# Performance work log

Hardware: AMD Instinct MI355X
Metric: run time of the kernel (lower is better)

## Reference

```python
import jax, jax.numpy as jnp
import numpy as np

DIM = 1024
EPS = 1e-5


def setup_inputs() -> dict:
    key = jax.random.key(0)
    ks = jax.random.split(key, 7)
    C = DIM
    x = jax.random.normal(ks[0], (4, 4096, C), dtype=jnp.float32)
    norm_w = jnp.ones((C,), dtype=jnp.float32)
    norm_b = jnp.zeros((C,), dtype=jnp.float32)
    s = 1.0 / np.sqrt(C)
    qkv_w = jax.random.uniform(ks[1], (3 * C, C), dtype=jnp.float32, minval=-s, maxval=s)
    qkv_b = jax.random.uniform(ks[2], (3 * C,), dtype=jnp.float32, minval=-s, maxval=s)
    proj_w = jax.random.uniform(ks[3], (C, C), dtype=jnp.float32, minval=-s, maxval=s)
    proj_b = jax.random.uniform(ks[4], (C,), dtype=jnp.float32, minval=-s, maxval=s)
    return {"x": x, "norm_w": norm_w, "norm_b": norm_b, "qkv_w": qkv_w,
            "qkv_b": qkv_b, "proj_w": proj_w, "proj_b": proj_b}


def _layernorm(x, w, b):
    mu = jnp.mean(x, axis=-1, keepdims=True)
    var = jnp.mean(jnp.square(x - mu), axis=-1, keepdims=True)
    return (x - mu) * jax.lax.rsqrt(var + EPS) * w + b


def reference(x, norm_w, norm_b, qkv_w, qkv_b, proj_w, proj_b):
    B, T, C = x.shape
    residual = x
    h = _layernorm(x, norm_w, norm_b)
    qkv = jnp.einsum('btc,oc->bto', h, qkv_w) + qkv_b  # [B,T,3C]
    q, k, v = qkv[..., :C], qkv[..., C:2 * C], qkv[..., 2 * C:]
    attn = jnp.einsum('btc,bsc->bts', q, k) / jnp.sqrt(jnp.float32(C))  # raw QK^T, no softmax
    o = jnp.einsum('bts,bsc->btc', attn, v)
    o = jnp.einsum('btc,oc->bto', o, proj_w) + proj_b
    return residual + o  # dropout is identity in eval mode
```

## Files before the change

### kernel.cpp

```cpp
#include <hip/hip_runtime.h>

typedef _Float16 f16;
typedef _Float16 f16x4 __attribute__((ext_vector_type(4)));
typedef _Float16 f16x8 __attribute__((ext_vector_type(8)));
typedef float f32x4 __attribute__((ext_vector_type(4)));

#define AS1 __attribute__((address_space(1)))
#define AS3 __attribute__((address_space(3)))

__device__ __forceinline__ void gl_lds16(const f16* g, f16* l) {
  __builtin_amdgcn_global_load_lds((const AS1 void*)g, (AS3 void*)l, 16, 0, 0);
}

__global__ __launch_bounds__(256) void ln_kernel(const float* __restrict__ x,
                                                 const float* __restrict__ gw,
                                                 const float* __restrict__ gb,
                                                 f16* __restrict__ H) {
  const int wv = threadIdx.x >> 6, lane = threadIdx.x & 63;
  const long row = (long)blockIdx.x * 4 + wv;
  const float* xr = x + row * 1024;
  float4 v[4];
  float s = 0.f, s2 = 0.f;
#pragma unroll
  for (int j = 0; j < 4; ++j) {
    v[j] = ((const float4*)xr)[lane + 64 * j];
    s  += v[j].x + v[j].y + v[j].z + v[j].w;
    s2 += v[j].x * v[j].x + v[j].y * v[j].y + v[j].z * v[j].z + v[j].w * v[j].w;
  }
#pragma unroll
  for (int off = 32; off > 0; off >>= 1) {
    s  += __shfl_xor(s, off);
    s2 += __shfl_xor(s2, off);
  }
  const float mu = s * (1.0f / 1024.0f);
  const float rstd = rsqrtf(s2 * (1.0f / 1024.0f) - mu * mu + 1e-5f);
#pragma unroll
  for (int j = 0; j < 4; ++j) {
    const float4 w4 = ((const float4*)gw)[lane + 64 * j];
    const float4 b4 = ((const float4*)gb)[lane + 64 * j];
    f16x4 h;
    h[0] = (f16)((v[j].x - mu) * rstd * w4.x + b4.x);
    h[1] = (f16)((v[j].y - mu) * rstd * w4.y + b4.y);
    h[2] = (f16)((v[j].z - mu) * rstd * w4.z + b4.z);
    h[3] = (f16)((v[j].w - mu) * rstd * w4.w + b4.w);
    *(f16x4*)(H + row * 1024 + (lane + 64 * j) * 4) = h;
  }
}

__global__ __launch_bounds__(256) void transpose_cs_kernel(const f16* __restrict__ H,
                                                           f16* __restrict__ Ht,
                                                           float* __restrict__ hs) {
  __shared__ f16 tile[64][68];
  __shared__ float csum[4][64];
  const int b = blockIdx.z;
  const long Hb  = (long)b * 4096 * 1024;
  const long Htb = (long)b * 1024 * 4096;
  const int t0 = blockIdx.y * 64, c0 = blockIdx.x * 64;
  const int tid = threadIdx.x;
  const int r = tid >> 2, g0 = tid & 3;
#pragma unroll
  for (int i = 0; i < 4; ++i) {
    const int g = g0 + i * 4;
    f16x4 v = *(const f16x4*)(H + Hb + (long)(t0 + r) * 1024 + c0 + g * 4);
    *(f16x4*)&tile[r][g * 4] = v;
  }
  __syncthreads();
  {
    const int cl = tid & 63, rg = tid >> 6;
    float s = 0.f;
#pragma unroll
    for (int rr = 0; rr < 16; ++rr) s += (float)tile[rg * 16 + rr][cl];
    csum[rg][cl] = s;
  }
#pragma unroll
  for (int i = 0; i < 4; ++i) {
    const int g = g0 + i * 4;
    f16x4 v;
    v[0] = tile[g * 4 + 0][r];
    v[1] = tile[g * 4 + 1][r];
    v[2] = tile[g * 4 + 2][r];
    v[3] = tile[g * 4 + 3][r];
    *(f16x4*)(Ht + Htb + (long)(c0 + r) * 4096 + t0 + g * 4) = v;
  }
  __syncthreads();
  if (tid < 64)
    atomicAdd(&hs[b * 1024 + c0 + tid],
              csum[0][tid] + csum[1][tid] + csum[2][tid] + csum[3][tid]);
}

__global__ __launch_bounds__(256) void transcast4(const float* __restrict__ qkv_w,
                                                  const float* __restrict__ proj_w,
                                                  f16* __restrict__ WT3,
                                                  f16* __restrict__ Wh,
                                                  f16* __restrict__ Ph) {
  const int z = blockIdx.z;
  __shared__ f16 tile[64][68];
  const int r0 = blockIdx.y * 64, c0 = blockIdx.x * 64;
  const int tid = threadIdx.x;
  const int r = tid >> 2, g0 = tid & 3;
  if (z == 3) {
#pragma unroll
    for (int i = 0; i < 4; ++i) {
      const int g = g0 + i * 4;
      float4 v = *(const float4*)(proj_w + (long)(r0 + r) * 1024 + c0 + g * 4);
      f16x4 h; h[0]=(f16)v.x; h[1]=(f16)v.y; h[2]=(f16)v.z; h[3]=(f16)v.w;
      *(f16x4*)(Ph + (long)(r0 + r) * 1024 + c0 + g * 4) = h;
    }
    return;
  }
  const float* W = qkv_w + (long)z * 1048576;
  f16* WT = WT3 + (long)z * 1048576;
#pragma unroll
  for (int i = 0; i < 4; ++i) {
    const int g = g0 + i * 4;
    float4 v = *(const float4*)(W + (long)(r0 + r) * 1024 + c0 + g * 4);
    f16x4 h; h[0]=(f16)v.x; h[1]=(f16)v.y; h[2]=(f16)v.z; h[3]=(f16)v.w;
    *(f16x4*)&tile[r][g * 4] = h;
    if (z >= 1)
      *(f16x4*)(Wh + (long)z * 1048576 + (long)(r0 + r) * 1024 + c0 + g * 4) = h;
  }
  __syncthreads();
#pragma unroll
  for (int i = 0; i < 4; ++i) {
    const int g = g0 + i * 4;
    f16x4 v;
    v[0] = tile[g * 4 + 0][r];
    v[1] = tile[g * 4 + 1][r];
    v[2] = tile[g * 4 + 2][r];
    v[3] = tile[g * 4 + 3][r];
    *(f16x4*)(WT + (long)(c0 + r) * 1024 + r0 + g * 4) = v;
  }
}

__device__ __forceinline__ float dot1024(const f16* __restrict__ row,
                                         const float* __restrict__ v) {
  const int lane = threadIdx.x & 63;
  float s = 0.f;
#pragma unroll
  for (int j = 0; j < 2; ++j) {
    const int d = (lane + 64 * j) * 8;
    f16x8 a = *(const f16x8*)(row + d);
    float4 h0 = *(const float4*)(v + d);
    float4 h1 = *(const float4*)(v + d + 4);
    s += (float)a[0] * h0.x + (float)a[1] * h0.y + (float)a[2] * h0.z + (float)a[3] * h0.w
       + (float)a[4] * h1.x + (float)a[5] * h1.y + (float)a[6] * h1.z + (float)a[7] * h1.w;
  }
#pragma unroll
  for (int off = 32; off > 0; off >>= 1) s += __shfl_down(s, off);
  return s;
}

__device__ __forceinline__ float dotf1024(const float* __restrict__ a,
                                          const float* __restrict__ v) {
  const int lane = threadIdx.x & 63;
  float s = 0.f;
#pragma unroll
  for (int j = 0; j < 4; ++j) {
    const int d = (lane + 64 * j) * 4;
    float4 x = *(const float4*)(a + d);
    float4 q = *(const float4*)(v + d);
    s += x.x * q.x + x.y * q.y + x.z * q.z + x.w * q.w;
  }
#pragma unroll
  for (int off = 32; off > 0; off >>= 1) s += __shfl_down(s, off);
  return s;
}

__global__ void gemv3a(const f16* __restrict__ WT3, const f16* __restrict__ Ph,
                       const float* __restrict__ qkv_b, float* __restrict__ ayd,
                       float* __restrict__ scal) {
  if (blockIdx.x == 3072) {
    float s = dotf1024(qkv_b + 1024, qkv_b);
    if ((threadIdx.x & 63) == 0) scal[4] = s;
    return;
  }
  const int which = blockIdx.x >> 10, m = blockIdx.x & 1023;
  const f16* row;
  const float* v;
  if (which == 0)      { row = WT3 + (long)m * 1024;            v = qkv_b + 1024; }
  else if (which == 1) { row = WT3 + 1048576 + (long)m * 1024;  v = qkv_b; }
  else                 { row = Ph + (long)m * 1024;             v = qkv_b + 2048; }
  float s = dot1024(row, v);
  if ((threadIdx.x & 63) == 0) ayd[which * 1024 + m] = s;
}

__global__ void gemv3b(const f16* __restrict__ U, const f16* __restrict__ PWv,
                       const f16* __restrict__ Gh, const float* __restrict__ hs,
                       const float* __restrict__ ayd, float* __restrict__ efz,
                       float* __restrict__ scal) {
  if (blockIdx.x >= 12288) {
    const int b = blockIdx.x - 12288;
    float s = dotf1024(hs + b * 1024, ayd + 1024);
    if ((threadIdx.x & 63) == 0) scal[b] = s;
    return;
  }
  const int sel = blockIdx.x >> 12, r = blockIdx.x & 4095;
  const int b = r >> 10, m = r & 1023;
  const f16* row;
  const float* v;
  if (sel == 0)      { row = U + (long)m * 1024;                       v = hs + b * 1024; }
  else if (sel == 1) { row = PWv + (long)m * 1024;                     v = hs + b * 1024; }
  else               { row = Gh + (long)b * 1048576 + (long)m * 1024;  v = ayd + 1024; }
  float s = dot1024(row, v);
  if ((threadIdx.x & 63) == 0) efz[sel * 4096 + r] = s;
}

__global__ void gemvC2n(const f16* __restrict__ PWv, const float* __restrict__ efz,
                        const float* __restrict__ ayd, const float* __restrict__ scal,
                        const float* __restrict__ proj_b, float* __restrict__ c2) {
  const int b = blockIdx.x >> 10, c = blockIdx.x & 1023;
  float s = dot1024(PWv + (long)c * 1024, efz + 8192 + b * 1024);
  if ((threadIdx.x & 63) == 0) {
    const float d = ayd[2048 + c];
    c2[b * 1024 + c] = (s + d * scal[b] + scal[4] * (efz[4096 + b * 1024 + c] + 4096.f * d))
                         * 0.03125f + proj_b[c];
  }
}

#define GP64_COMMON()                                        \
  const int tid = threadIdx.x;                               \
  const int wave = tid >> 6, lane = tid & 63;                \
  const int lr = lane & 15, lk = lane >> 4;                  \
  const int srow = tid >> 3;                                 \
  const int slc  = (tid & 7) ^ (srow & 7);                   \
  const int kc0 = ((lk) ^ (lr & 7)) * 8;                     \
  const int kc1 = ((4 + lk) ^ (lr & 7)) * 8;

#define GEMM_WAIT8(NBUF_, r_)                                               \
  do {                                                                      \
    if constexpr (NBUF_ == 3) {                                             \
      if ((r_) >= 2)      asm volatile("s_waitcnt vmcnt(16)" ::: "memory"); \
      else if ((r_) == 1) asm volatile("s_waitcnt vmcnt(8)" ::: "memory");  \
      else                asm volatile("s_waitcnt vmcnt(0)" ::: "memory");  \
    } else {                                                                \
      if ((r_) >= 1)      asm volatile("s_waitcnt vmcnt(8)" ::: "memory");  \
      else                asm volatile("s_waitcnt vmcnt(0)" ::: "memory");  \
    }                                                                       \
  } while (0)

#define COMP64_HALF(asb_, bsb_, kc_)                                             \
  do {                                                                           \
    const f16* asb = (asb_);                                                     \
    const f16* bsb = (bsb_);                                                     \
    f16x8 af[4], bf[4];                                                          \
    _Pragma("unroll")                                                            \
    for (int mi = 0; mi < 4; ++mi)                                               \
      af[mi] = *(const f16x8*)(asb + (wm * 64 + mi * 16 + lr) * 64 + (kc_));     \
    _Pragma("unroll")                                                            \
    for (int ni = 0; ni < 4; ++ni)                                               \
      bf[ni] = *(const f16x8*)(bsb + (wn * 64 + ni * 16 + lr) * 64 + (kc_));     \
    _Pragma("unroll")                                                            \
    for (int mi = 0; mi < 4; ++mi)                                               \
      _Pragma("unroll")                                                          \
      for (int ni = 0; ni < 4; ++ni)                                             \
        acc[mi][ni] = __builtin_amdgcn_mfma_f32_16x16x32_f16(af[mi], bf[ni],     \
                                                             acc[mi][ni], 0, 0, 0); \
  } while (0)

#define GEMM_BODY_LOOP(NBUF_, NT_, STAGEM)                       \
  do {                                                           \
    if constexpr (NBUF_ == 3) {                                  \
      STAGEM(0, 0); STAGEM(1, 1);                                \
      int cur = 0, stg = 2;                                      \
      for (int t = 0; t < (NT_); ++t) {                          \
        if (t + 2 < (NT_)) STAGEM(stg, t + 2);                   \
        GEMM_WAIT8(3, (NT_) - 1 - t);                            \
        asm volatile("s_barrier" ::: "memory");                  \
        __builtin_amdgcn_s_setprio(1);                           \
        COMP64_HALF(&As[cur][0], &Bs[cur][0], kc0);              \
        COMP64_HALF(&As[cur][0], &Bs[cur][0], kc1);              \
        __builtin_amdgcn_s_setprio(0);                           \
        asm volatile("s_waitcnt lgkmcnt(0)" ::: "memory");       \
        asm volatile("s_barrier" ::: "memory");                  \
        cur = (cur + 1 == 3) ? 0 : cur + 1;                      \
        stg = (stg + 1 == 3) ? 0 : stg + 1;                      \
      }                                                          \
    } else {                                                     \
      STAGEM(0, 0);                                              \
      int cur = 0;                                               \
      for (int t = 0; t < (NT_); ++t) {                          \
        if (t + 1 < (NT_)) STAGEM(cur ^ 1, t + 1);               \
        GEMM_WAIT8(2, (NT_) - 1 - t);                            \
        asm volatile("s_barrier" ::: "memory");                  \
        __builtin_amdgcn_s_setprio(1);                           \
        COMP64_HALF(&As[cur][0], &Bs[cur][0], kc0);              \
        COMP64_HALF(&As[cur][0], &Bs[cur][0], kc1);              \
        __builtin_amdgcn_s_setprio(0);                           \
        asm volatile("s_waitcnt lgkmcnt(0)" ::: "memory");       \
        asm volatile("s_barrier" ::: "memory");                  \
        cur ^= 1;                                                \
      }                                                          \
    }                                                            \
  } while (0)

template <int MODE>
__global__ __launch_bounds__(256) void gemm128(
    const f16* __restrict__ A, const f16* __restrict__ B, int K,
    long sA, long sB, long sC,
    f16* __restrict__ Ch,
    const float* __restrict__ dvec, const float* __restrict__ evec,
    const float* __restrict__ fvec, const float* __restrict__ avec) {
  const int b = blockIdx.z;
  A += (long)b * sA;
  B += (long)b * sB;
  const int nx = blockIdx.y & 7;
  const int ny = blockIdx.x;

  GP64_COMMON();
  const int wm = wave >> 1, wn = wave & 1;

  __shared__ __align__(16) f16 As[3][8192];
  __shared__ __align__(16) f16 Bs[3][8192];

  const long aoffs = (long)(ny * 128 + srow) * K + slc * 8;
  const long boffs = (long)(nx * 128 + srow) * K + slc * 8;

  f32x4 zero = {0.f, 0.f, 0.f, 0.f};
  f32x4 acc[4][4];
#pragma unroll
  for (int mi = 0; mi < 4; ++mi)
#pragma unroll
    for (int ni = 0; ni < 4; ++ni) acc[mi][ni] = zero;

#define STAGE(buf, kt)                                                              \
  do {                                                                              \
    f16* asb = &As[buf][0];                                                         \
    f16* bsb = &Bs[buf][0];                                                         \
    _Pragma("unroll")                                                               \
    for (int q = 0; q < 4; ++q) {                                                   \
      gl_lds16(A + aoffs + (long)q * 32 * K + (kt) * 64, asb + q * 2048 + tid * 8); \
      gl_lds16(B + boffs + (long)q * 32 * K + (kt) * 64, bsb + q * 2048 + tid * 8); \
    }                                                                               \
  } while (0)

  const int nt = K >> 6;
  GEMM_BODY_LOOP(3, nt, STAGE);
#undef STAGE

  const long cb = (long)b * sC;
  const int m0 = ny * 128 + wm * 64;
  const int n0 = nx * 128 + wn * 64;
#pragma unroll
  for (int mi = 0; mi < 4; ++mi)
#pragma unroll
    for (int ni = 0; ni < 4; ++ni)
#pragma unroll
      for (int j = 0; j < 4; ++j) {
        const int gm = m0 + mi * 16 + lk * 4 + j;
        const int gn = n0 + ni * 16 + lr;
        float val = acc[mi][ni][j];
        if constexpr (MODE == 0) {
          Ch[cb + (long)gm * 1024 + gn] = (f16)val;
        } else {
          const float dm = dvec[gm];
          const float fm = fvec[b * 1024 + gm];
          const float en = evec[b * 1024 + gn];
          const float an = avec[gn];
          val = (val + dm * en + (fm + 4096.f * dm) * an) * 0.03125f;
          Ch[cb + (long)gm * 1024 + gn] = (f16)val;
        }
      }
}

__global__ __launch_bounds__(256) void gemmGUV(const f16* __restrict__ Ht,
                                               const f16* __restrict__ WT3,
                                               const f16* __restrict__ Ph,
                                               f16* __restrict__ part,
                                               f16* __restrict__ U,
                                               f16* __restrict__ PWv) {
  GP64_COMMON();
  const int wm = wave >> 1, wn = wave & 1;

  __shared__ __align__(16) f16 As[2][8192];
  __shared__ __align__(16) f16 Bs[2][8192];

  const int bid = blockIdx.x;
  const f16 *Ab, *Bb;
  long rs;
  int tileid = 0, zz = 0, selt = 0;
  if (bid < 576) {
    tileid = bid % 36;
    zz = bid / 36;
    const int b = zz & 3, ks4 = zz >> 2;
    int ti = 0, trem = tileid;
    while (trem >= 8 - ti) { trem -= 8 - ti; ++ti; }
    const int tj = ti + trem;
    const f16* Hb = Ht + (long)b * 4194304;
    rs = 4096;
    Ab = Hb + (long)(ti * 128 + srow) * 4096 + (long)ks4 * 1024 + slc * 8;
    Bb = Hb + (long)(tj * 128 + srow) * 4096 + (long)ks4 * 1024 + slc * 8;
  } else {
    const int u = bid - 576;
    selt = (u >> 6) + 1;
    const int t = u & 63;
    const int ny = t >> 3, nxx = t & 7;
    const f16* A0 = (selt == 2) ? Ph : WT3;
    const f16* B0 = (selt == 2) ? (WT3 + 2097152) : (WT3 + 1048576);
    rs = 1024;
    Ab = A0 + (long)(ny * 128 + srow) * 1024 + slc * 8;
    Bb = B0 + (long)(nxx * 128 + srow) * 1024 + slc * 8;
  }

  f32x4 zero = {0.f, 0.f, 0.f, 0.f};
  f32x4 acc[4][4];
#pragma unroll
  for (int mi = 0; mi < 4; ++mi)
#pragma unroll
    for (int ni = 0; ni < 4; ++ni) acc[mi][ni] = zero;

#define STAGE(buf, kt)                                                            \
  do {                                                                            \
    f16* asb = &As[buf][0];                                                       \
    f16* bsb = &Bs[buf][0];                                                       \
    _Pragma("unroll")                                                             \
    for (int q = 0; q < 4; ++q) {                                                 \
      gl_lds16(Ab + (long)q * 32 * rs + (kt) * 64, asb + q * 2048 + tid * 8);     \
      gl_lds16(Bb + (long)q * 32 * rs + (kt) * 64, bsb + q * 2048 + tid * 8);     \
    }                                                                             \
  } while (0)

  GEMM_BODY_LOOP(2, 16, STAGE);
#undef STAGE

  if (selt == 0) {
    f16* P = part + ((long)zz * 36 + tileid) * 16384;
#pragma unroll
    for (int mi = 0; mi < 4; ++mi)
#pragma unroll
      for (int ni = 0; ni < 4; ++ni)
#pragma unroll
        for (int j = 0; j < 4; ++j) {
          const int gm = wm * 64 + mi * 16 + lk * 4 + j;
          const int gn = wn * 64 + ni * 16 + lr;
          P[gm * 128 + gn] = (f16)acc[mi][ni][j];
        }
  } else {
    const int u = bid - 576;
    const int t = u & 63;
    const int ny = t >> 3, nxx = t & 7;
    f16* C = (selt == 2) ? PWv : U;
    const int m0 = ny * 128 + wm * 64;
    const int n0 = nxx * 128 + wn * 64;
#pragma unroll
    for (int mi = 0; mi < 4; ++mi)
#pragma unroll
      for (int ni = 0; ni < 4; ++ni)
#pragma unroll
        for (int j = 0; j < 4; ++j) {
          const int gm = m0 + mi * 16 + lk * 4 + j;
          const int gn = n0 + ni * 16 + lr;
          C[(long)gm * 1024 + gn] = (f16)acc[mi][ni][j];
        }
  }
}

__global__ __launch_bounds__(512) void gemm256f(
    const f16* __restrict__ A,
    const f16* __restrict__ Bw,
    const float* __restrict__ resid,
    const float* __restrict__ c2v,
    float* __restrict__ outF) {
  const int lin = blockIdx.y * 4 + blockIdx.x;
  const int xcd = lin & 7, slot = lin >> 3;
  const int ny = xcd * 8 + (slot >> 2);
  const int nx = slot & 3;
  const int bb = ny >> 4;

  GP64_COMMON();
  const int wm = wave >> 2, wn = wave & 3;

  __shared__ __align__(16) f16 As[2][16384];
  __shared__ __align__(16) f16 Bs[2][16384];

  const f16* Ab = A + (long)ny * 262144;
  const f16* Bb = Bw + (long)bb * 1048576 + (long)nx * 262144;
  const long offs = (long)srow * 1024 + slc * 8;

  f32x4 zero = {0.f, 0.f, 0.f, 0.f};
  f32x4 acc[8][4];
#pragma unroll
  for (int mi = 0; mi < 8; ++mi)
#pragma unroll
    for (int ni = 0; ni < 4; ++ni) acc[mi][ni] = zero;

#define STAGE(buf, kt)                                                             \
  do {                                                                             \
    f16* asb = &As[buf][0];                                                        \
    f16* bsb = &Bs[buf][0];                                                        \
    _Pragma("unroll")                                                              \
    for (int q = 0; q < 4; ++q) {                                                  \
      gl_lds16(Ab + offs + (long)q * 65536 + (kt) * 64, asb + q * 4096 + tid * 8); \
      gl_lds16(Bb + offs + (long)q * 65536 + (kt) * 64, bsb + q * 4096 + tid * 8); \
    }                                                                              \
  } while (0)

  const int nt = 16;
  STAGE(0, 0);
  int cur = 0;
  for (int t = 0; t < nt; ++t) {
    if (t + 1 < nt) STAGE(cur ^ 1, t + 1);
    GEMM_WAIT8(2, nt - 1 - t);
    asm volatile("s_barrier" ::: "memory");
    __builtin_amdgcn_s_setprio(1);
#pragma unroll
    for (int ks = 0; ks < 2; ++ks) {
      const int kc = ks ? kc1 : kc0;
      const f16* asb = &As[cur][0];
      const f16* bsb = &Bs[cur][0];
      f16x8 af[8], bf[4];
#pragma unroll
      for (int mi = 0; mi < 8; ++mi)
        af[mi] = *(const f16x8*)(asb + (wm * 128 + mi * 16 + lr) * 64 + kc);
#pragma unroll
      for (int ni = 0; ni < 4; ++ni)
        bf[ni] = *(const f16x8*)(bsb + (wn * 64 + ni * 16 + lr) * 64 + kc);
#pragma unroll
      for (int mi = 0; mi < 8; ++mi)
#pragma unroll
        for (int ni = 0; ni < 4; ++ni)
          acc[mi][ni] = __builtin_amdgcn_mfma_f32_16x16x32_f16(af[mi], bf[ni],
                                                               acc[mi][ni], 0, 0, 0);
    }
    __builtin_amdgcn_s_setprio(0);
    asm volatile("s_waitcnt lgkmcnt(0)" ::: "memory");
    asm volatile("s_barrier" ::: "memory");
    cur ^= 1;
  }
#undef STAGE

  float* weps = ((float*)&As[0][0]) + wave * 1088;
  const int m0 = ny * 256 + wm * 128;
  const int n0 = nx * 256 + wn * 64;
  const int err = lane >> 3;
  const int ecc = (lane & 7) * 4;
  float4 cc2[2];
#pragma unroll
  for (int q = 0; q < 2; ++q)
    cc2[q] = *(const float4*)&c2v[bb * 1024 + n0 + ecc + 32 * q];

#pragma unroll
  for (int mi = 0; mi < 8; ++mi) {
#pragma unroll
    for (int ni = 0; ni < 4; ++ni)
#pragma unroll
      for (int j = 0; j < 4; ++j)
        weps[(lk * 4 + j) * 68 + ni * 16 + lr] = acc[mi][ni][j];
    asm volatile("s_waitcnt lgkmcnt(0)" ::: "memory");
#pragma unroll
    for (int h = 0; h < 2; ++h)
#pragma unroll
      for (int q = 0; q < 2; ++q) {
        const int rr = err + 8 * h;
        const int cc = ecc + 32 * q;
        float4 o = *(const float4*)&weps[rr * 68 + cc];
        const long gbase = (long)(m0 + mi * 16 + rr) * 1024 + n0 + cc;
        const float4 rv = *(const float4*)&resid[gbase];
        float4 ov;
        ov.x = o.x + rv.x + cc2[q].x;
        ov.y = o.y + rv.y + cc2[q].y;
        ov.z = o.z + rv.z + cc2[q].z;
        ov.w = o.w + rv.w + cc2[q].w;
        *(float4*)&outF[gbase] = ov;
      }
  }
}

__global__ __launch_bounds__(256) void treduce(const f16* __restrict__ part,
                                               f16* __restrict__ Gh) {
  const int tileid = blockIdx.x, b = blockIdx.y;
  int ti = 0, trem = tileid;
  while (trem >= 8 - ti) { trem -= 8 - ti; ++ti; }
  const int tj = ti + trem;
  __shared__ f16 tl[128][132];
  const int tid = threadIdx.x;
  f16* Gb = Gh + (long)b * 1048576;
  const long pbase = ((long)b * 36 + tileid) * 16384;
#pragma unroll
  for (int it = 0; it < 16; ++it) {
    const int e = it * 1024 + tid * 4;
    const int r = e >> 7, c = e & 127;
    f16x4 p0 = *(const f16x4*)(part + pbase + e);
    f16x4 p1 = *(const f16x4*)(part + pbase + 2359296 + e);
    f16x4 p2 = *(const f16x4*)(part + pbase + 4718592 + e);
    f16x4 p3 = *(const f16x4*)(part + pbase + 7077888 + e);
    f16x4 sv;
#pragma unroll
    for (int j = 0; j < 4; ++j)
      sv[j] = (f16)((float)p0[j] + (float)p1[j] + (float)p2[j] + (float)p3[j]);
    *(f16x4*)(Gb + (long)(ti * 128 + r) * 1024 + tj * 128 + c) = sv;
    *(f16x4*)&tl[r][c] = sv;
  }
  if (ti != tj) {
    __syncthreads();
#pragma unroll
    for (int it = 0; it < 16; ++it) {
      const int e = it * 1024 + tid * 4;
      const int r = e >> 7, c = e & 127;
      f16x4 v;
      v[0] = tl[c + 0][r];
      v[1] = tl[c + 1][r];
      v[2] = tl[c + 2][r];
      v[3] = tl[c + 3][r];
      *(f16x4*)(Gb + (long)(tj * 128 + r) * 1024 + ti * 128 + c) = v;
    }
  }
}

extern "C" void kernel_launch(void* const* d_in, const int* in_sizes, int n_in,
                              void* d_out, int out_size, void* d_ws, size_t ws_size,
                              hipStream_t stream) {
  const float* x      = (const float*)d_in[0];
  const float* norm_w = (const float*)d_in[1];
  const float* norm_b = (const float*)d_in[2];
  const float* qkv_w  = (const float*)d_in[3];
  const float* qkv_b  = (const float*)d_in[4];
  const float* proj_w = (const float*)d_in[5];
  const float* proj_b = (const float*)d_in[6];
  float* out = (float*)d_out;
  char* ws = (char*)d_ws;

  const size_t OFF_H    = 0;
  const size_t OFF_HT   = 33554432;
  const size_t OFF_T1   = 33554432;
  const size_t OFF_T2   = 41943040;
  const size_t OFF_WH   = 67108864;
  const size_t OFF_PH   = 73400320;
  const size_t OFF_WT3  = 75497472;
  const size_t OFF_U    = 81788928;
  const size_t OFF_PWV  = 83886080;
  const size_t OFF_GH   = 85983232;
  const size_t OFF_PART = 94371840;
  const size_t OFF_HS   = 115343360;
  const size_t OFF_AYD  = 115392512;
  const size_t OFF_SCAL = 115404800;
  const size_t OFF_EFZ  = 115405824;
  const size_t OFF_C2   = 115471360;

  f16* H    = (f16*)(ws + OFF_H);
  f16* Ht   = (f16*)(ws + OFF_HT);
  f16* T1   = (f16*)(ws + OFF_T1);
  f16* T2   = (f16*)(ws + OFF_T2);
  f16* Wh   = (f16*)(ws + OFF_WH);
  f16* Ph   = (f16*)(ws + OFF_PH);
  f16* WT3  = (f16*)(ws + OFF_WT3);
  f16* U    = (f16*)(ws + OFF_U);
  f16* PWv  = (f16*)(ws + OFF_PWV);
  f16* Gh   = (f16*)(ws + OFF_GH);
  f16* part = (f16*)(ws + OFF_PART);
  float* hs   = (float*)(ws + OFF_HS);
  float* ayd  = (float*)(ws + OFF_AYD);
  float* scal = (float*)(ws + OFF_SCAL);
  float* efz  = (float*)(ws + OFF_EFZ);
  float* c2v  = (float*)(ws + OFF_C2);

  transcast4<<<dim3(16, 16, 4), 256, 0, stream>>>(qkv_w, proj_w, WT3, Wh, Ph);
  gemv3a<<<dim3(3073), 64, 0, stream>>>(WT3, Ph, qkv_b, ayd, scal);

  ln_kernel<<<dim3(4096), 256, 0, stream>>>(x, norm_w, norm_b, H);
  hipMemsetAsync(ws + OFF_HS, 0, 16384, stream);
  transpose_cs_kernel<<<dim3(16, 64, 4), 256, 0, stream>>>(H, Ht, hs);

  gemmGUV<<<dim3(704), 256, 0, stream>>>(Ht, WT3, Ph, part, U, PWv);
  treduce<<<dim3(36, 4), 256, 0, stream>>>(part, Gh);

  gemv3b<<<dim3(12292), 64, 0, stream>>>(U, PWv, Gh, hs, ayd, efz, scal);
  gemvC2n<<<dim3(4096), 64, 0, stream>>>(PWv, efz, ayd, scal, proj_b, c2v);

  gemm128<0><<<dim3(8, 8, 4), 256, 0, stream>>>(U, Gh, 1024, 0L, 1048576L, 1048576L,
      T1, nullptr, nullptr, nullptr, nullptr);
  gemm128<1><<<dim3(8, 8, 4), 256, 0, stream>>>(PWv, T1, 1024, 0L, 1048576L, 1048576L,
      T2, ayd + 2048, efz, efz + 4096, ayd);

  gemm256f<<<dim3(4, 64), 512, 0, stream>>>(H, T2, x, c2v, out);
}
```

Measured before the change: 201.8 us.

## Interleave global-to-LDS prefetch with MFMA phases in 256x256 GEMM loop

Splits each k-tile iteration of the 256x256 fp16 GEMM into four phases. Each phase reads a half of the A fragments (and B fragments when needed), issues a slice of the next tile's global_load_lds, then runs 16 MFMAs. The goal is to spread memory traffic across the compute and cut register pressure by holding only 4 A fragments instead of 8. In exchange it adds several barriers and vmcnt waits per iteration, and the wait counts must match the order of the loads exactly.

```diff
diff --git a/kernel.cpp b/kernel.cpp
--- a/kernel.cpp
+++ b/kernel.cpp
@@ -483,50 +483,80 @@
 #pragma unroll
     for (int ni = 0; ni < 4; ++ni) acc[mi][ni] = zero;
 
-#define STAGE(buf, kt)                                                             \
-  do {                                                                             \
-    f16* asb = &As[buf][0];                                                        \
-    f16* bsb = &Bs[buf][0];                                                        \
-    _Pragma("unroll")                                                              \
-    for (int q = 0; q < 4; ++q) {                                                  \
-      gl_lds16(Ab + offs + (long)q * 65536 + (kt) * 64, asb + q * 4096 + tid * 8); \
-      gl_lds16(Bb + offs + (long)q * 65536 + (kt) * 64, bsb + q * 4096 + tid * 8); \
-    }                                                                              \
-  } while (0)
+#define SA(buf, kt, q) gl_lds16(Ab + offs + (long)(q) * 65536 + (kt) * 64, &As[buf][(q) * 4096] + tid * 8)
+#define SB(buf, kt, q) gl_lds16(Bb + offs + (long)(q) * 65536 + (kt) * 64, &Bs[buf][(q) * 4096] + tid * 8)
+
+#define RD_BF(dst, bsb, kc)                                                       \
+  _Pragma("unroll")                                                               \
+  for (int ni = 0; ni < 4; ++ni)                                                  \
+    dst[ni] = *(const f16x8*)((bsb) + (wn * 64 + ni * 16 + lr) * 64 + (kc));
+#define RD_AF(dst, asb, mh, kc)                                                   \
+  _Pragma("unroll")                                                               \
+  for (int mi = 0; mi < 4; ++mi)                                                  \
+    dst[mi] = *(const f16x8*)((asb) + (wm * 128 + (mh) * 64 + mi * 16 + lr) * 64 + (kc));
+#define MF16(af_, bf_, mo)                                                        \
+  __builtin_amdgcn_s_setprio(1);                                                  \
+  _Pragma("unroll")                                                               \
+  for (int mi = 0; mi < 4; ++mi)                                                  \
+    _Pragma("unroll")                                                             \
+    for (int ni = 0; ni < 4; ++ni)                                                \
+      acc[(mo) + mi][ni] = __builtin_amdgcn_mfma_f32_16x16x32_f16(af_[mi], bf_[ni], \
+                                                                  acc[(mo) + mi][ni], 0, 0, 0); \
+  __builtin_amdgcn_s_setprio(0);
 
   const int nt = 16;
-  STAGE(0, 0);
+  SB(0, 0, 0); SB(0, 0, 1); SB(0, 0, 2); SB(0, 0, 3);
+  SA(0, 0, 0); SA(0, 0, 2); SA(0, 0, 1); SA(0, 0, 3);
+
   int cur = 0;
   for (int t = 0; t < nt; ++t) {
-    if (t + 1 < nt) STAGE(cur ^ 1, t + 1);
-    GEMM_WAIT8(2, nt - 1 - t);
+    const f16* asb = &As[cur][0];
+    const f16* bsb = &Bs[cur][0];
+    const int nb = cur ^ 1;
+    const bool st = (t + 1 < nt);
+    f16x8 bf[4], af[4];
+
+    asm volatile("s_waitcnt vmcnt(2)" ::: "memory");
     asm volatile("s_barrier" ::: "memory");
-    __builtin_amdgcn_s_setprio(1);
-#pragma unroll
-    for (int ks = 0; ks < 2; ++ks) {
-      const int kc = ks ? kc1 : kc0;
-      const f16* asb = &As[cur][0];
-      const f16* bsb = &Bs[cur][0];
-      f16x8 af[8], bf[4];
-#pragma unroll
-      for (int mi = 0; mi < 8; ++mi)
-        af[mi] = *(const f16x8*)(asb + (wm * 128 + mi * 16 + lr) * 64 + kc);
-#pragma unroll
-      for (int ni = 0; ni < 4; ++ni)
-        bf[ni] = *(const f16x8*)(bsb + (wn * 64 + ni * 16 + lr) * 64 + kc);
-#pragma unroll
-      for (int mi = 0; mi < 8; ++mi)
-#pragma unroll
-        for (int ni = 0; ni < 4; ++ni)
-          acc[mi][ni] = __builtin_amdgcn_mfma_f32_16x16x32_f16(af[mi], bf[ni],
-                                                               acc[mi][ni], 0, 0, 0);
-    }
-    __builtin_amdgcn_s_setprio(0);
+    RD_BF(bf, bsb, kc0);
+    RD_AF(af, asb, 0, kc0);
+    if (st) { SB(nb, t + 1, 0); SB(nb, t + 1, 1); }
     asm volatile("s_waitcnt lgkmcnt(0)" ::: "memory");
+    MF16(af, bf, 0);
     asm volatile("s_barrier" ::: "memory");
+
+    if (st) asm volatile("s_waitcnt vmcnt(2)" ::: "memory");
+    else    asm volatile("s_waitcnt vmcnt(0)" ::: "memory");
+    asm volatile("s_barrier" ::: "memory");
+    RD_AF(af, asb, 1, kc0);
+    if (st) { SB(nb, t + 1, 2); SB(nb, t + 1, 3); }
+    asm volatile("s_waitcnt lgkmcnt(0)" ::: "memory");
+    MF16(af, bf, 4);
+    asm volatile("s_barrier" ::: "memory");
+
+    RD_BF(bf, bsb, kc1);
+    RD_AF(af, asb, 0, kc1);
+    if (st) { SA(nb, t + 1, 0); SA(nb, t + 1, 2); }
+    asm volatile("s_waitcnt lgkmcnt(0)" ::: "memory");
+    MF16(af, bf, 0);
+    asm volatile("s_barrier" ::: "memory");
+
+    RD_AF(af, asb, 1, kc1);
+    if (st) { SA(nb, t + 1, 1); SA(nb, t + 1, 3); }
+    asm volatile("s_waitcnt lgkmcnt(0)" ::: "memory");
+    MF16(af, bf, 4);
+    asm volatile("s_barrier" ::: "memory");
+
     cur ^= 1;
   }
-#undef STAGE
+#undef SA
+#undef SB
+#undef RD_BF
+#undef RD_AF
+#undef MF16
+
+  asm volatile("s_waitcnt vmcnt(0)" ::: "memory");
+  asm volatile("s_barrier" ::: "memory");
 
   float* weps = ((float*)&As[0][0]) + wave * 1088;
   const int m0 = ny * 256 + wm * 128;
```

Measured after the change: 203.6 us. No clear change (+0.9%).
